# Kernel optimization log

Measured on AMD Instinct MI355X. Metric: run time of the kernel, lower is better.

The kernel has to match this reference:

```python
import jax, jax.numpy as jnp
import numpy as np

N, M, FIN, FOUT, K_CHEB, NNZ = 8, 50000, 16, 32, 4, 800000


def setup_inputs() -> dict:
    key = jax.random.key(0)
    k1, k2, k3, k4, k5 = jax.random.split(key, 5)
    x = jax.random.normal(k1, (N, M, FIN), dtype=jnp.float32)
    l_row = jax.random.randint(k2, (NNZ,), 0, M, dtype=jnp.int32)
    l_col = jax.random.randint(k3, (NNZ,), 0, M, dtype=jnp.int32)
    # values of the rescaled (lmax=2) Laplacian; small scale keeps recurrence stable
    l_vals = jax.random.normal(k4, (NNZ,), dtype=jnp.float32) * 0.05
    w = jax.random.normal(k5, (FIN, K_CHEB, FOUT), dtype=jnp.float32) * (1.0 / np.sqrt(FIN * K_CHEB))
    b = jnp.zeros((1, 1, FOUT), dtype=jnp.float32)
    return {"x": x, "l_vals": l_vals, "w": w, "b": b, "l_row": l_row, "l_col": l_col}


def reference(x, l_vals, w, b, l_row, l_col):
    n, m, fin = x.shape
    k_cheb = w.shape[1]
    # X0: [M, Fin*N], matching tf.transpose(inputs,[1,2,0]) + reshape
    X0 = jnp.transpose(x, (1, 2, 0)).reshape(m, fin * n)

    def spmm(X):  # sparse L (COO) @ dense X via gather + segment-sum
        return jax.ops.segment_sum(l_vals[:, None] * X[l_col], l_row, num_segments=m)

    terms = [X0]
    if k_cheb > 1:
        X1 = spmm(X0)
        terms.append(X1)
        for _ in range(2, k_cheb):
            X2 = 2.0 * spmm(X1) - X0  # Chebyshev recurrence T_k = 2 L T_{k-1} - T_{k-2}
            terms.append(X2)
            X0, X1 = X1, X2

    Xs = jnp.stack(terms, axis=0).reshape(k_cheb, m, fin, n)  # [K, M, Fin, N]
    Xs = jnp.transpose(Xs, (3, 1, 2, 0))                      # [N, M, Fin, K]
    return jnp.einsum('nmfk,fko->nmo', Xs, w) + b
```

## Files before the change

### kernel.cpp

```cpp
#include <hip/hip_runtime.h>

constexpr int N_    = 8;
constexpr int M_    = 50000;
constexpr int FIN_  = 16;
constexpr int FOUT_ = 32;
constexpr int KCH_  = 4;
constexpr int NNZ_  = 800000;
constexpr int ROWB_ = 128;
constexpr int SCAN_NB = (M_ + 255) / 256;
constexpr int RPB16_ = 16;
constexpr int NBKT_  = (M_ + 255) / 256;
constexpr int BSC_BLOCKS_ = 256;
constexpr int CHUNK_ = NNZ_ / BSC_BLOCKS_;
constexpr int NTILE_ = M_ / 2;


typedef float f32x4 __attribute__((ext_vector_type(4)));
typedef unsigned short u16x8 __attribute__((ext_vector_type(8)));
typedef short bf16x8 __attribute__((ext_vector_type(8)));
typedef float f32x4v __attribute__((ext_vector_type(4)));

__device__ __forceinline__ float bf2f(unsigned short u) {
    return __uint_as_float(((unsigned int)u) << 16);
}
__device__ __forceinline__ unsigned short f2bf(float f) {
    unsigned int u = __float_as_uint(f);
    return (unsigned short)((u + 0x7fffu + ((u >> 16) & 1u)) >> 16);
}

__global__ void k_zero(int4* __restrict__ p, int n4) {
    int i = blockIdx.x * blockDim.x + threadIdx.x;
    if (i < n4) p[i] = make_int4(0, 0, 0, 0);
}

__global__ void k_build_x0(const float* __restrict__ x, unsigned short* __restrict__ t0) {
    int t = blockIdx.x * blockDim.x + threadIdx.x;
    if (t >= M_ * ROWB_) return;
    int f = t & 15;
    int n = (t >> 4) & 7;
    int m = t >> 7;
    t0[t] = f2bf(x[((size_t)n * M_ + m) * FIN_ + f]);
}

__global__ void k_hist(const int* __restrict__ row, int* __restrict__ cnt) {
    int i = blockIdx.x * blockDim.x + threadIdx.x;
    if (i < NNZ_) atomicAdd(&cnt[row[i]], 1);
}

__global__ void k_blocksum(const int* __restrict__ cnt, int* __restrict__ bsum) {
    __shared__ int s[256];
    int t = threadIdx.x;
    int idx = blockIdx.x * 256 + t;
    s[t] = (idx < M_) ? cnt[idx] : 0;
    __syncthreads();
    for (int off = 128; off > 0; off >>= 1) {
        if (t < off) s[t] += s[t + off];
        __syncthreads();
    }
    if (t == 0) bsum[blockIdx.x] = s[0];
}

__global__ void k_scan_bsum(const int* __restrict__ bsum, int* __restrict__ boff) {
    __shared__ int s[256];
    int t = threadIdx.x;
    int v = (t < SCAN_NB) ? bsum[t] : 0;
    s[t] = v;
    __syncthreads();
    for (int off = 1; off < 256; off <<= 1) {
        int a = (t >= off) ? s[t - off] : 0;
        __syncthreads();
        s[t] += a;
        __syncthreads();
    }
    if (t < SCAN_NB) boff[t] = s[t] - v;
}

__global__ void k_emit(const int* __restrict__ cnt, const int* __restrict__ boff,
                       int* __restrict__ row_ptr) {
    __shared__ int s[256];
    int t = threadIdx.x;
    int idx = blockIdx.x * 256 + t;
    int v = (idx < M_) ? cnt[idx] : 0;
    s[t] = v;
    __syncthreads();
    for (int off = 1; off < 256; off <<= 1) {
        int a = (t >= off) ? s[t - off] : 0;
        __syncthreads();
        s[t] += a;
        __syncthreads();
    }
    if (idx < M_) row_ptr[idx] = boff[blockIdx.x] + s[t] - v;
    if (idx == 0) row_ptr[M_] = NNZ_;
}

__global__ void k_binit(const int* __restrict__ row_ptr, int* __restrict__ bticket) {
    int b = blockIdx.x * blockDim.x + threadIdx.x;
    if (b < NBKT_) bticket[b] = row_ptr[b * 256];
}

__global__ __launch_bounds__(256) void k_bscatter(
        const float* __restrict__ vals, const int* __restrict__ row,
        const int* __restrict__ col, int* __restrict__ bticket,
        int2* __restrict__ stage) {
    __shared__ int cnt[NBKT_];
    __shared__ int base[NBKT_];
    const int t = threadIdx.x;
    const int i0 = blockIdx.x * CHUNK_;
    for (int b = t; b < NBKT_; b += 256) cnt[b] = 0;
    __syncthreads();
    for (int i = i0 + t; i < i0 + CHUNK_; i += 256)
        atomicAdd(&cnt[row[i] >> 8], 1);
    __syncthreads();
    for (int b = t; b < NBKT_; b += 256) {
        base[b] = (cnt[b] > 0) ? atomicAdd(&bticket[b], cnt[b]) : 0;
        cnt[b] = 0;
    }
    __syncthreads();
    for (int i = i0 + t; i < i0 + CHUNK_; i += 256) {
        const int r = row[i];
        const int b = r >> 8;
        const int k = atomicAdd(&cnt[b], 1);
        stage[base[b] + k] = make_int2(__float_as_int(vals[i]),
                                       col[i] | ((r & 255) << 16));
    }
}

__global__ __launch_bounds__(256) void k_bsort(
        const int* __restrict__ row_ptr, const int2* __restrict__ stage,
        int2* __restrict__ pairs) {
    __shared__ int rp_loc[257];
    __shared__ int c2[256];
    const int b  = blockIdx.x;
    const int t  = threadIdx.x;
    const int r0 = b * 256;
    const int nr = (r0 + 256 <= M_) ? 256 : (M_ - r0);
    if (t < nr) rp_loc[t] = row_ptr[r0 + t];
    if (t == 0) rp_loc[nr] = row_ptr[r0 + nr];
    c2[t] = 0;
    __syncthreads();
    const int base = rp_loc[0];
    const int end  = rp_loc[nr];
    for (int e = base + t; e < end; e += 256) {
        const int2 en = stage[e];
        const int rl = en.y >> 16;
        const int k  = atomicAdd(&c2[rl], 1);
        pairs[rp_loc[rl] + k] = make_int2(en.x, en.y & 0xFFFF);
    }
}

__global__ __launch_bounds__(256) void k_spmm_bf16(
        const unsigned short* __restrict__ X, const unsigned short* __restrict__ prev,
        unsigned short* __restrict__ Y, const int* __restrict__ rp,
        const long long* __restrict__ pairs, float scale) {
    const int r = blockIdx.x * RPB16_ + (threadIdx.x >> 4);
    if (r >= M_) return;
    const int lane = threadIdx.x & 15;
    const unsigned short* Xl = X + lane * 8;
    const size_t off = (size_t)r * ROWB_ + lane * 8;

    const int jb = rp[r], je = rp[r + 1];
    f32x4 slo0 = {0,0,0,0}, shi0 = {0,0,0,0};
    f32x4 slo1 = {0,0,0,0}, shi1 = {0,0,0,0};
    f32x4 slo2 = {0,0,0,0}, shi2 = {0,0,0,0};
    f32x4 slo3 = {0,0,0,0}, shi3 = {0,0,0,0};
    int j = jb;
    for (; j + 3 < je; j += 4) {
        const long long p0 = pairs[j],     p1 = pairs[j + 1];
        const long long p2 = pairs[j + 2], p3 = pairs[j + 3];
        const float v0 = __int_as_float((int)p0);
        const float v1 = __int_as_float((int)p1);
        const float v2 = __int_as_float((int)p2);
        const float v3 = __int_as_float((int)p3);
        const u16x8 u0 = *reinterpret_cast<const u16x8*>(Xl + (size_t)((int)(p0 >> 32)) * ROWB_);
        const u16x8 u1 = *reinterpret_cast<const u16x8*>(Xl + (size_t)((int)(p1 >> 32)) * ROWB_);
        const u16x8 u2 = *reinterpret_cast<const u16x8*>(Xl + (size_t)((int)(p2 >> 32)) * ROWB_);
        const u16x8 u3 = *reinterpret_cast<const u16x8*>(Xl + (size_t)((int)(p3 >> 32)) * ROWB_);
        slo0 += v0 * (f32x4){bf2f(u0[0]), bf2f(u0[1]), bf2f(u0[2]), bf2f(u0[3])};
        shi0 += v0 * (f32x4){bf2f(u0[4]), bf2f(u0[5]), bf2f(u0[6]), bf2f(u0[7])};
        slo1 += v1 * (f32x4){bf2f(u1[0]), bf2f(u1[1]), bf2f(u1[2]), bf2f(u1[3])};
        shi1 += v1 * (f32x4){bf2f(u1[4]), bf2f(u1[5]), bf2f(u1[6]), bf2f(u1[7])};
        slo2 += v2 * (f32x4){bf2f(u2[0]), bf2f(u2[1]), bf2f(u2[2]), bf2f(u2[3])};
        shi2 += v2 * (f32x4){bf2f(u2[4]), bf2f(u2[5]), bf2f(u2[6]), bf2f(u2[7])};
        slo3 += v3 * (f32x4){bf2f(u3[0]), bf2f(u3[1]), bf2f(u3[2]), bf2f(u3[3])};
        shi3 += v3 * (f32x4){bf2f(u3[4]), bf2f(u3[5]), bf2f(u3[6]), bf2f(u3[7])};
    }
    for (; j < je; ++j) {
        const long long p0 = pairs[j];
        const float v0 = __int_as_float((int)p0);
        const u16x8 u0 = *reinterpret_cast<const u16x8*>(Xl + (size_t)((int)(p0 >> 32)) * ROWB_);
        slo0 += v0 * (f32x4){bf2f(u0[0]), bf2f(u0[1]), bf2f(u0[2]), bf2f(u0[3])};
        shi0 += v0 * (f32x4){bf2f(u0[4]), bf2f(u0[5]), bf2f(u0[6]), bf2f(u0[7])};
    }
    f32x4 rlo = scale * ((slo0 + slo1) + (slo2 + slo3));
    f32x4 rhi = scale * ((shi0 + shi1) + (shi2 + shi3));
    if (prev) {
        const u16x8 pv = *reinterpret_cast<const u16x8*>(prev + off);
        rlo -= (f32x4){bf2f(pv[0]), bf2f(pv[1]), bf2f(pv[2]), bf2f(pv[3])};
        rhi -= (f32x4){bf2f(pv[4]), bf2f(pv[5]), bf2f(pv[6]), bf2f(pv[7])};
    }
    u16x8 o;
    o[0] = f2bf(rlo.x); o[1] = f2bf(rlo.y); o[2] = f2bf(rlo.z); o[3] = f2bf(rlo.w);
    o[4] = f2bf(rhi.x); o[5] = f2bf(rhi.y); o[6] = f2bf(rhi.z); o[7] = f2bf(rhi.w);
    *reinterpret_cast<u16x8*>(Y + off) = o;
}

__global__ __launch_bounds__(256) void k_final(
        const unsigned short* __restrict__ T0, const unsigned short* __restrict__ T1,
        const unsigned short* __restrict__ T2, const unsigned short* __restrict__ T3,
        const float* __restrict__ w, const float* __restrict__ b,
        float* __restrict__ out) {
    const int lane = threadIdx.x & 63;
    const int lg   = lane >> 4;
    const int ll   = lane & 15;
    const int wid    = (blockIdx.x * blockDim.x + threadIdx.x) >> 6;
    const int nwaves = (gridDim.x * blockDim.x) >> 6;

    bf16x8 bfrag[2][2];
#pragma unroll
    for (int mm = 0; mm < 2; ++mm)
#pragma unroll
        for (int oh = 0; oh < 2; ++oh)
#pragma unroll
            for (int j = 0; j < 8; ++j) {
                const int k  = lg * 8 + j;
                const int kc = mm * 2 + (k >> 4);
                const int f  = k & 15;
                bfrag[mm][oh][j] =
                    (short)f2bf(w[(f * KCH_ + kc) * FOUT_ + oh * 16 + ll]);
            }
    const float bias0 = b[ll], bias1 = b[16 + ll];

    const unsigned short* TA = (lg < 2) ? T0 : T1;
    const unsigned short* TB = (lg < 2) ? T2 : T3;
    const int mloc = ll >> 3;
    const int n    = ll & 7;
    const int fofs = (lg & 1) * 8;
    const size_t eoff = (size_t)n * 16 + fofs;

    for (int tile = wid; tile < NTILE_; tile += nwaves) {
        const int m0 = tile * 2;
        const size_t rowoff = (size_t)(m0 + mloc) * ROWB_ + eoff;
        const bf16x8 a01 = *reinterpret_cast<const bf16x8*>(TA + rowoff);
        const bf16x8 a23 = *reinterpret_cast<const bf16x8*>(TB + rowoff);

        f32x4v acc0 = {bias0, bias0, bias0, bias0};
        f32x4v acc1 = {bias1, bias1, bias1, bias1};
        acc0 = __builtin_amdgcn_mfma_f32_16x16x32_bf16(a01, bfrag[0][0], acc0, 0, 0, 0);
        acc0 = __builtin_amdgcn_mfma_f32_16x16x32_bf16(a23, bfrag[1][0], acc0, 0, 0, 0);
        acc1 = __builtin_amdgcn_mfma_f32_16x16x32_bf16(a01, bfrag[0][1], acc1, 0, 0, 0);
        acc1 = __builtin_amdgcn_mfma_f32_16x16x32_bf16(a23, bfrag[1][1], acc1, 0, 0, 0);

#pragma unroll
        for (int r = 0; r < 4; ++r) {
            const int drow = lg * 4 + r;
            const int dm   = drow >> 3;
            const int dn   = drow & 7;
            float* base = out + ((size_t)dn * M_ + m0 + dm) * FOUT_;
            base[ll]      = acc0[r];
            base[16 + ll] = acc1[r];
        }
    }
}

__global__ __launch_bounds__(256) void k_accum(
        const unsigned short* __restrict__ T, const float* __restrict__ w,
        const float* __restrict__ b, float* __restrict__ out, int k, int init) {
    int t = blockIdx.x * blockDim.x + threadIdx.x;
    if (t >= M_ * N_) return;
    const int n = t & 7;
    const int m = t >> 3;

    float* base = out + ((size_t)n * M_ + m) * FOUT_;
    float4 acc[8];
#pragma unroll
    for (int o4 = 0; o4 < 8; ++o4)
        acc[o4] = init ? *reinterpret_cast<const float4*>(b + o4 * 4)
                       : *reinterpret_cast<const float4*>(base + o4 * 4);

    const unsigned short* tk = T + (size_t)m * ROWB_ + n * 16;
    const u16x8 lo = *reinterpret_cast<const u16x8*>(tk);
    const u16x8 hi = *reinterpret_cast<const u16x8*>(tk + 8);
#pragma unroll
    for (int f = 0; f < FIN_; ++f) {
        const float tv = bf2f(f < 8 ? lo[f] : hi[f - 8]);
        const float* wr = w + (f * KCH_ + k) * FOUT_;
#pragma unroll
        for (int o4 = 0; o4 < 8; ++o4) {
            float4 wv = *reinterpret_cast<const float4*>(wr + o4 * 4);
            acc[o4].x += tv * wv.x; acc[o4].y += tv * wv.y;
            acc[o4].z += tv * wv.z; acc[o4].w += tv * wv.w;
        }
    }
#pragma unroll
    for (int o4 = 0; o4 < 8; ++o4)
        *reinterpret_cast<float4*>(base + o4 * 4) = acc[o4];
}

extern "C" void kernel_launch(void* const* d_in, const int* in_sizes, int n_in,
                              void* d_out, int out_size, void* d_ws, size_t ws_size,
                              hipStream_t stream) {
    const float* x    = (const float*)d_in[0];
    const float* vals = (const float*)d_in[1];
    const float* w    = (const float*)d_in[2];
    const float* b    = (const float*)d_in[3];
    const int*   row  = (const int*)d_in[4];
    const int*   col  = (const int*)d_in[5];
    float* out = (float*)d_out;

    const size_t tElems = (size_t)M_ * ROWB_;
    const size_t tBytes = tElems * 2;
    const size_t csrBytes = (size_t)(M_ + 1) * 4 + (size_t)M_ * 4
                          + 2 * (size_t)NNZ_ * 8 + 4096;
    const size_t fusedBytes = 4 * tBytes + csrBytes;
    const bool fused = ws_size >= fusedBytes;

    unsigned short* X0 = (unsigned short*)d_ws;
    unsigned short* T1 = X0 + tElems;
    unsigned short* T2 = T1 + tElems;
    unsigned short* T3 = fused ? (T2 + tElems) : T1;
    char* p = (char*)(fused ? (T3 + tElems) : (T2 + tElems));
    int2* pairs   = (int2*)p;              p += (size_t)NNZ_ * 8;
    int2* stage   = (int2*)p;              p += (size_t)NNZ_ * 8;
    int*  row_ptr = (int*)p;               p += (size_t)(M_ + 1) * 4;
    int*  cnt     = (int*)p;               p += (size_t)M_ * 4;
    int*  bsum    = (int*)p;               p += 1024;
    int*  boff    = (int*)p;               p += 1024;
    int*  bticket = (int*)p;

    const int TB = 256;
    dim3 blk(TB);
    dim3 gN((NNZ_ + TB - 1) / TB);
    dim3 gX((M_ * ROWB_ + TB - 1) / TB);
    dim3 gS((M_ + RPB16_ - 1) / RPB16_);
    dim3 gFM(1024);
    dim3 gF((M_ * N_ + TB - 1) / TB);
    dim3 gZ((M_ / 4 + TB - 1) / TB);

    hipLaunchKernelGGL(k_zero,      gZ, blk, 0, stream, (int4*)cnt, M_ / 4);
    hipLaunchKernelGGL(k_hist,      gN, blk, 0, stream, row, cnt);
    hipLaunchKernelGGL(k_blocksum,  dim3(SCAN_NB), blk, 0, stream, cnt, bsum);
    hipLaunchKernelGGL(k_scan_bsum, dim3(1), blk, 0, stream, bsum, boff);
    hipLaunchKernelGGL(k_emit,      dim3(SCAN_NB), blk, 0, stream, cnt, boff, row_ptr);

    hipLaunchKernelGGL(k_binit,    dim3(1), blk, 0, stream, row_ptr, bticket);
    hipLaunchKernelGGL(k_bscatter, dim3(BSC_BLOCKS_), blk, 0, stream,
                       vals, row, col, bticket, stage);
    hipLaunchKernelGGL(k_bsort,    dim3(NBKT_), blk, 0, stream, row_ptr, stage, pairs);

    hipLaunchKernelGGL(k_build_x0, gX, blk, 0, stream, x, X0);

    const long long* pr = (const long long*)pairs;
    if (fused) {
        hipLaunchKernelGGL(k_spmm_bf16, gS, blk, 0, stream, X0, (const unsigned short*)nullptr,
                           T1, row_ptr, pr, 1.0f);
        hipLaunchKernelGGL(k_spmm_bf16, gS, blk, 0, stream, T1, X0, T2, row_ptr, pr, 2.0f);
        hipLaunchKernelGGL(k_spmm_bf16, gS, blk, 0, stream, T2, T1, T3, row_ptr, pr, 2.0f);
        hipLaunchKernelGGL(k_final, gFM, blk, 0, stream, X0, T1, T2, T3, w, b, out);
    } else {
        hipLaunchKernelGGL(k_accum, gF, blk, 0, stream, X0, w, b, out, 0, 1);
        hipLaunchKernelGGL(k_spmm_bf16, gS, blk, 0, stream, X0, (const unsigned short*)nullptr,
                           T1, row_ptr, pr, 1.0f);
        hipLaunchKernelGGL(k_accum, gF, blk, 0, stream, T1, w, b, out, 1, 0);
        hipLaunchKernelGGL(k_spmm_bf16, gS, blk, 0, stream, T1, X0, T2, row_ptr, pr, 2.0f);
        hipLaunchKernelGGL(k_accum, gF, blk, 0, stream, T2, w, b, out, 2, 0);
        hipLaunchKernelGGL(k_spmm_bf16, gS, blk, 0, stream, T2, T1, T1, row_ptr, pr, 2.0f);
        hipLaunchKernelGGL(k_accum, gF, blk, 0, stream, T1, w, b, out, 3, 0);
    }
}
```

Before: 206.4 us.

## Build CSR via bucket-level histogram and compute row pointers inside bucket sort

Replaces the per-row global atomic histogram plus the three-kernel row scan with a shared-memory bucket histogram (256-row buckets) and a single-block bucket scan. Per-row offsets are now computed inside k_bsort by counting and scanning the bucket's staged entries locally, and row_ptr is written there. This removes 800k global atomics and several kernel launches. In exchange, k_bsort reads the staged entries twice.

```diff
diff --git a/kernel.cpp b/kernel.cpp
--- a/kernel.cpp
+++ b/kernel.cpp
@@ -7,7 +7,6 @@
 constexpr int KCH_  = 4;
 constexpr int NNZ_  = 800000;
 constexpr int ROWB_ = 128;
-constexpr int SCAN_NB = (M_ + 255) / 256;
 constexpr int RPB16_ = 16;
 constexpr int NBKT_  = (M_ + 255) / 256;
 constexpr int BSC_BLOCKS_ = 256;
@@ -28,9 +27,9 @@
     return (unsigned short)((u + 0x7fffu + ((u >> 16) & 1u)) >> 16);
 }
 
-__global__ void k_zero(int4* __restrict__ p, int n4) {
+__global__ void k_zero_small(int* __restrict__ p, int n) {
     int i = blockIdx.x * blockDim.x + threadIdx.x;
-    if (i < n4) p[i] = make_int4(0, 0, 0, 0);
+    if (i < n) p[i] = 0;
 }
 
 __global__ void k_build_x0(const float* __restrict__ x, unsigned short* __restrict__ t0) {
@@ -42,28 +41,25 @@
     t0[t] = f2bf(x[((size_t)n * M_ + m) * FIN_ + f]);
 }
 
-__global__ void k_hist(const int* __restrict__ row, int* __restrict__ cnt) {
-    int i = blockIdx.x * blockDim.x + threadIdx.x;
-    if (i < NNZ_) atomicAdd(&cnt[row[i]], 1);
-}
-
-__global__ void k_blocksum(const int* __restrict__ cnt, int* __restrict__ bsum) {
+__global__ __launch_bounds__(256) void k_bhist(const int* __restrict__ row,
+                                               int* __restrict__ bcnt) {
+    __shared__ int cnt[NBKT_];
+    const int t = threadIdx.x;
+    for (int b = t; b < NBKT_; b += 256) cnt[b] = 0;
+    __syncthreads();
+    const int i0 = blockIdx.x * CHUNK_;
+    for (int i = i0 + t; i < i0 + CHUNK_; i += 256)
+        atomicAdd(&cnt[row[i] >> 8], 1);
+    __syncthreads();
+    for (int b = t; b < NBKT_; b += 256)
+        if (cnt[b]) atomicAdd(&bcnt[b], cnt[b]);
+}
+
+__global__ void k_bscan(const int* __restrict__ bcnt, int* __restrict__ bbase,
+                        int* __restrict__ bticket, int* __restrict__ row_ptr) {
     __shared__ int s[256];
-    int t = threadIdx.x;
-    int idx = blockIdx.x * 256 + t;
-    s[t] = (idx < M_) ? cnt[idx] : 0;
-    __syncthreads();
-    for (int off = 128; off > 0; off >>= 1) {
-        if (t < off) s[t] += s[t + off];
-        __syncthreads();
-    }
-    if (t == 0) bsum[blockIdx.x] = s[0];
-}
-
-__global__ void k_scan_bsum(const int* __restrict__ bsum, int* __restrict__ boff) {
-    __shared__ int s[256];
-    int t = threadIdx.x;
-    int v = (t < SCAN_NB) ? bsum[t] : 0;
+    const int t = threadIdx.x;
+    const int v = (t < NBKT_) ? bcnt[t] : 0;
     s[t] = v;
     __syncthreads();
     for (int off = 1; off < 256; off <<= 1) {
@@ -72,30 +68,12 @@
         s[t] += a;
         __syncthreads();
     }
-    if (t < SCAN_NB) boff[t] = s[t] - v;
-}
-
-__global__ void k_emit(const int* __restrict__ cnt, const int* __restrict__ boff,
-                       int* __restrict__ row_ptr) {
-    __shared__ int s[256];
-    int t = threadIdx.x;
-    int idx = blockIdx.x * 256 + t;
-    int v = (idx < M_) ? cnt[idx] : 0;
-    s[t] = v;
-    __syncthreads();
-    for (int off = 1; off < 256; off <<= 1) {
-        int a = (t >= off) ? s[t - off] : 0;
-        __syncthreads();
-        s[t] += a;
-        __syncthreads();
-    }
-    if (idx < M_) row_ptr[idx] = boff[blockIdx.x] + s[t] - v;
-    if (idx == 0) row_ptr[M_] = NNZ_;
-}
-
-__global__ void k_binit(const int* __restrict__ row_ptr, int* __restrict__ bticket) {
-    int b = blockIdx.x * blockDim.x + threadIdx.x;
-    if (b < NBKT_) bticket[b] = row_ptr[b * 256];
+    if (t < NBKT_) {
+        const int e = s[t] - v;
+        bbase[t]   = e;
+        bticket[t] = e;
+    }
+    if (t == 0) { bbase[NBKT_] = NNZ_; row_ptr[M_] = NNZ_; }
 }
 
 __global__ __launch_bounds__(256) void k_bscatter(
@@ -126,25 +104,40 @@
 }
 
 __global__ __launch_bounds__(256) void k_bsort(
-        const int* __restrict__ row_ptr, const int2* __restrict__ stage,
-        int2* __restrict__ pairs) {
-    __shared__ int rp_loc[257];
+        const int* __restrict__ bbase, const int2* __restrict__ stage,
+        int2* __restrict__ pairs, int* __restrict__ row_ptr) {
     __shared__ int c2[256];
+    __shared__ int s[256];
+    __shared__ int rloc[256];
     const int b  = blockIdx.x;
     const int t  = threadIdx.x;
     const int r0 = b * 256;
     const int nr = (r0 + 256 <= M_) ? 256 : (M_ - r0);
-    if (t < nr) rp_loc[t] = row_ptr[r0 + t];
-    if (t == 0) rp_loc[nr] = row_ptr[r0 + nr];
+    const int base = bbase[b];
+    const int end  = bbase[b + 1];
     c2[t] = 0;
     __syncthreads();
-    const int base = rp_loc[0];
-    const int end  = rp_loc[nr];
+    for (int e = base + t; e < end; e += 256)
+        atomicAdd(&c2[stage[e].y >> 16], 1);
+    __syncthreads();
+    const int v = c2[t];
+    s[t] = v;
+    __syncthreads();
+    for (int off = 1; off < 256; off <<= 1) {
+        int a = (t >= off) ? s[t - off] : 0;
+        __syncthreads();
+        s[t] += a;
+        __syncthreads();
+    }
+    rloc[t] = base + s[t] - v;
+    if (t < nr) row_ptr[r0 + t] = rloc[t];
+    c2[t] = 0;
+    __syncthreads();
     for (int e = base + t; e < end; e += 256) {
         const int2 en = stage[e];
         const int rl = en.y >> 16;
         const int k  = atomicAdd(&c2[rl], 1);
-        pairs[rp_loc[rl] + k] = make_int2(en.x, en.y & 0xFFFF);
+        pairs[rloc[rl] + k] = make_int2(en.x, en.y & 0xFFFF);
     }
 }
 
@@ -309,8 +302,8 @@
 
     const size_t tElems = (size_t)M_ * ROWB_;
     const size_t tBytes = tElems * 2;
-    const size_t csrBytes = (size_t)(M_ + 1) * 4 + (size_t)M_ * 4
-                          + 2 * (size_t)NNZ_ * 8 + 4096;
+    const size_t csrBytes = (size_t)(M_ + 1) * 4
+                          + 2 * (size_t)NNZ_ * 8 + 8192;
     const size_t fusedBytes = 4 * tBytes + csrBytes;
     const bool fused = ws_size >= fusedBytes;
 
@@ -322,30 +315,24 @@
     int2* pairs   = (int2*)p;              p += (size_t)NNZ_ * 8;
     int2* stage   = (int2*)p;              p += (size_t)NNZ_ * 8;
     int*  row_ptr = (int*)p;               p += (size_t)(M_ + 1) * 4;
-    int*  cnt     = (int*)p;               p += (size_t)M_ * 4;
-    int*  bsum    = (int*)p;               p += 1024;
-    int*  boff    = (int*)p;               p += 1024;
+    int*  bcnt    = (int*)p;               p += 1024;
+    int*  bbase   = (int*)p;               p += 1024;
     int*  bticket = (int*)p;
 
     const int TB = 256;
     dim3 blk(TB);
-    dim3 gN((NNZ_ + TB - 1) / TB);
     dim3 gX((M_ * ROWB_ + TB - 1) / TB);
     dim3 gS((M_ + RPB16_ - 1) / RPB16_);
     dim3 gFM(1024);
     dim3 gF((M_ * N_ + TB - 1) / TB);
-    dim3 gZ((M_ / 4 + TB - 1) / TB);
-
-    hipLaunchKernelGGL(k_zero,      gZ, blk, 0, stream, (int4*)cnt, M_ / 4);
-    hipLaunchKernelGGL(k_hist,      gN, blk, 0, stream, row, cnt);
-    hipLaunchKernelGGL(k_blocksum,  dim3(SCAN_NB), blk, 0, stream, cnt, bsum);
-    hipLaunchKernelGGL(k_scan_bsum, dim3(1), blk, 0, stream, bsum, boff);
-    hipLaunchKernelGGL(k_emit,      dim3(SCAN_NB), blk, 0, stream, cnt, boff, row_ptr);
-
-    hipLaunchKernelGGL(k_binit,    dim3(1), blk, 0, stream, row_ptr, bticket);
+
+    hipLaunchKernelGGL(k_zero_small, dim3(1), blk, 0, stream, bcnt, NBKT_);
+    hipLaunchKernelGGL(k_bhist,    dim3(BSC_BLOCKS_), blk, 0, stream, row, bcnt);
+    hipLaunchKernelGGL(k_bscan,    dim3(1), blk, 0, stream, bcnt, bbase, bticket, row_ptr);
     hipLaunchKernelGGL(k_bscatter, dim3(BSC_BLOCKS_), blk, 0, stream,
                        vals, row, col, bticket, stage);
-    hipLaunchKernelGGL(k_bsort,    dim3(NBKT_), blk, 0, stream, row_ptr, stage, pairs);
+    hipLaunchKernelGGL(k_bsort,    dim3(NBKT_), blk, 0, stream, bbase, stage,
+                       pairs, row_ptr);
 
     hipLaunchKernelGGL(k_build_x0, gX, blk, 0, stream, x, X0);
 
```

Result: faster. 175.4 us (-15.0%).
